# Performance work log

Hardware: AMD Instinct MI355X
Metric: run time of the kernel (lower is better)

## Reference

```python
import jax, jax.numpy as jnp
import numpy as np
import math

_B, _L, _D, _H = 4, 2048, 512, 8
_DH = _D // _H


def setup_inputs() -> dict:
    key = jax.random.key(0)
    ks = jax.random.split(key, 16)
    w_scale = 1.0 / math.sqrt(_D)
    def lin(kw, kb):
        W = jax.random.uniform(kw, (_D, _D), jnp.float32, -w_scale, w_scale)
        b = jax.random.uniform(kb, (_D,), jnp.float32, -w_scale, w_scale)
        return W, b
    Wq_w, Wq_b = lin(ks[0], ks[1])
    Wk_w, Wk_b = lin(ks[2], ks[3])
    Wv_w, Wv_b = lin(ks[4], ks[5])
    fc_w, fc_b = lin(ks[6], ks[7])
    Q = jax.random.normal(ks[8], (_B, _L, _D), jnp.float32)
    K = jax.random.normal(ks[9], (_B, _L, _D), jnp.float32)
    V = jax.random.normal(ks[10], (_B, _L, _D), jnp.float32)
    # E = torch.rand(L, DH): uniform [0,1), non-trainable buffer
    E = jax.random.uniform(ks[11], (_L, _DH), jnp.float32)
    # causal mask: True (1) where attention is disallowed -> gets -1e9
    mask = jnp.triu(jnp.ones((_L, _L), dtype=bool), k=1)[None, None]  # (1,1,L,L)
    return {"Q": Q, "K": K, "V": V, "mask": mask,
            "Wq_w": Wq_w, "Wq_b": Wq_b, "Wk_w": Wk_w, "Wk_b": Wk_b,
            "Wv_w": Wv_w, "Wv_b": Wv_b, "fc_w": fc_w, "fc_b": fc_b,
            "E": E, "H": _H}


def reference(Q, K, V, mask, Wq_w, Wq_b, Wk_w, Wk_b, Wv_w, Wv_b, fc_w, fc_b, E, H):
    B, Lq, D = Q.shape
    DH = D // H

    def proj(x, W, b):  # torch Linear: x @ W.T + b, then split heads -> (B,H,L,DH)
        y = x @ W.T + b
        return y.reshape(B, -1, H, DH).transpose(0, 2, 1, 3)

    q = proj(Q, Wq_w, Wq_b)
    k = proj(K, Wk_w, Wk_b)
    v = proj(V, Wv_w, Wv_b)
    Lk = k.shape[2]

    # _get_left_embedding: last Lq rows of E
    Eu = E[max(0, E.shape[0] - Lq):, :]            # (e, DH), e == Lq here
    e = Eu.shape[0]

    QE = jnp.einsum('bhld,ed->bhle', q, Eu)        # (B,H,Lq,e)
    # _qe_masking: keep QE[..., i, j] where j >= e-1-i (upper anti-triangle)
    i = jnp.arange(Lq)[:, None]
    j = jnp.arange(e)[None, :]
    keep = (i + j >= e - 1).astype(QE.dtype)
    QE = QE * keep

    # _skewing: pad one zero column, reshape, drop first row
    padded = jnp.pad(QE, ((0, 0), (0, 0), (0, 0), (1, 0)))   # (B,H,Lq,e+1)
    Srel = padded.reshape(B, H, e + 1, Lq)[:, :, 1:, :]      # (B,H,e,Lq)
    if Lk < Lq:
        Srel = Srel[:, :, :, :Lk]

    logits = (jnp.einsum('bhld,bhmd->bhlm', q, k) + Srel) / math.sqrt(DH)
    logits = logits + mask.astype(jnp.float32) * (-1e9)
    AW = jax.nn.softmax(logits, axis=-1)
    out = jnp.einsum('bhlm,bhmd->bhld', AW, v)               # (B,H,Lq,DH)
    out = out.transpose(0, 2, 1, 3).reshape(B, -1, D)        # (B,Lq,D)
    return out @ fc_w.T + fc_b
```

## Files before the change

### kernel.cpp

```cpp
#include <hip/hip_runtime.h>
#include <stdint.h>

typedef __bf16 bf16;
typedef float f32x4 __attribute__((ext_vector_type(4)));
typedef bf16 bf16x8 __attribute__((ext_vector_type(8)));
typedef bf16 bf16x4 __attribute__((ext_vector_type(4)));

#define MFMA16(a, b, c) __builtin_amdgcn_mfma_f32_16x16x32_bf16((a), (b), (c), 0, 0, 0)
#define EXP2F(x) __builtin_amdgcn_exp2f(x)

__device__ __forceinline__ void gll16(const void* g, void* l) {
  __builtin_amdgcn_global_load_lds((const __attribute__((address_space(1))) void*)g,
                                   (__attribute__((address_space(3))) void*)l, 16, 0, 0);
}

__global__ __launch_bounds__(256) void convert_all(
    const float4* __restrict__ Q, const float4* __restrict__ K, const float4* __restrict__ V,
    const float4* __restrict__ Wq, const float4* __restrict__ Wk, const float4* __restrict__ Wv,
    const float4* __restrict__ fcw, const float4* __restrict__ E,
    bf16x4* __restrict__ Xq, bf16x4* __restrict__ Xk, bf16x4* __restrict__ Xv,
    bf16x4* __restrict__ Wqb, bf16x4* __restrict__ Wkb, bf16x4* __restrict__ Wvb,
    bf16x4* __restrict__ fcb, bf16x4* __restrict__ Eb) {
  int i = blockIdx.x * 256 + threadIdx.x;
  const float4* s;
  bf16x4* d;
  int off;
  if (i < 1048576) { s = Q; d = Xq; off = i; }
  else if (i < 2097152) { s = K; d = Xk; off = i - 1048576; }
  else if (i < 3145728) { s = V; d = Xv; off = i - 2097152; }
  else if (i < 3211264) { s = Wq; d = Wqb; off = i - 3145728; }
  else if (i < 3276800) { s = Wk; d = Wkb; off = i - 3211264; }
  else if (i < 3342336) { s = Wv; d = Wvb; off = i - 3276800; }
  else if (i < 3407872) { s = fcw; d = fcb; off = i - 3342336; }
  else { s = E; d = Eb; off = i - 3407872; }
  float4 v = s[off];
  bf16x4 o;
  o[0] = (bf16)v.x; o[1] = (bf16)v.y; o[2] = (bf16)v.z; o[3] = (bf16)v.w;
  d[off] = o;
}

__device__ __forceinline__ void gemm_core64(const bf16* __restrict__ A,
                                            const bf16* __restrict__ Bt, bf16* ldsA,
                                            bf16* ldsB, int m0, int n0, f32x4 acc[4][2]) {
  const int t = threadIdx.x;
  const int lane = t & 63, w = t >> 6;
  const int l15 = lane & 15, quad = lane >> 4;
  const int wm = w >> 1, wn = w & 1;
#pragma unroll
  for (int i = 0; i < 4; i++)
#pragma unroll
    for (int j = 0; j < 2; j++) acc[i][j] = (f32x4){0.f, 0.f, 0.f, 0.f};

  const int r0 = t >> 2, c0 = (t & 3) ^ (r0 & 3);
  const int r1 = r0 + 64;

  int aoff[4], boff[2];
#pragma unroll
  for (int mt = 0; mt < 4; mt++) {
    int m = wm * 64 + mt * 16 + l15;
    aoff[mt] = (m << 6) + ((quad ^ (l15 & 3)) << 4);
  }
#pragma unroll
  for (int nt = 0; nt < 2; nt++) {
    int n = wn * 32 + nt * 16 + l15;
    boff[nt] = (n << 6) + ((quad ^ (l15 & 3)) << 4);
  }
  bf16* ldsA1 = ldsA + w * 512;
  bf16* ldsA2 = ldsA + 2048 + w * 512;
  bf16* ldsB1 = ldsB + w * 512;

  for (int kt = 0; kt < 512; kt += 32) {
    gll16(A + (size_t)(m0 + r0) * 512 + kt + c0 * 8, ldsA1);
    gll16(A + (size_t)(m0 + r1) * 512 + kt + c0 * 8, ldsA2);
    gll16(Bt + (size_t)(n0 + r0) * 512 + kt + c0 * 8, ldsB1);
    __syncthreads();
    bf16x8 af[4], bfr[2];
#pragma unroll
    for (int mt = 0; mt < 4; mt++) af[mt] = *(const bf16x8*)((const char*)ldsA + aoff[mt]);
#pragma unroll
    for (int nt = 0; nt < 2; nt++) bfr[nt] = *(const bf16x8*)((const char*)ldsB + boff[nt]);
#pragma unroll
    for (int mt = 0; mt < 4; mt++)
#pragma unroll
      for (int nt = 0; nt < 2; nt++)
        acc[mt][nt] = MFMA16(af[mt], bfr[nt], acc[mt][nt]);
    __syncthreads();
  }
}

__global__ __launch_bounds__(256) void proj_gemm(
    const bf16* __restrict__ Xq, const bf16* __restrict__ Xk, const bf16* __restrict__ Xv,
    const bf16* __restrict__ Wq, const bf16* __restrict__ Wk, const bf16* __restrict__ Wv,
    const float* __restrict__ bq, const float* __restrict__ bk, const float* __restrict__ bv,
    bf16* __restrict__ qb, bf16* __restrict__ kb, bf16* __restrict__ vT) {
  __shared__ __align__(16) char smem[17408];
  bf16* ldsA = (bf16*)smem;
  bf16* ldsB = (bf16*)(smem + 8192);
  const int z = blockIdx.z;
  const bf16* A = z == 0 ? Xq : (z == 1 ? Xk : Xv);
  const bf16* W = z == 0 ? Wq : (z == 1 ? Wk : Wv);
  const float* bias = z == 0 ? bq : (z == 1 ? bk : bv);
  const int m0 = blockIdx.x * 128, n0 = blockIdx.y * 64;
  f32x4 acc[4][2];
  gemm_core64(A, W, ldsA, ldsB, m0, n0, acc);

  const int t = threadIdx.x;
  const int lane = t & 63, w = t >> 6;
  const int l15 = lane & 15, quad = lane >> 4;
  const int wm = w >> 1, wn = w & 1;
  if (z == 2) {
    bf16* T = (bf16*)smem;
    const int b = m0 >> 11, l0 = m0 & 2047, h0 = blockIdx.y;
#pragma unroll
    for (int mt = 0; mt < 4; mt++)
#pragma unroll
      for (int nt = 0; nt < 2; nt++) {
        int d = wn * 32 + nt * 16 + l15;
        int lloc = wm * 64 + mt * 16 + quad * 4;
        float bi = bias[n0 + d];
        bf16x4 pv;
#pragma unroll
        for (int r = 0; r < 4; r++) pv[r] = (bf16)(acc[mt][nt][r] + bi);
        *(bf16x4*)&T[d * 136 + lloc] = pv;
      }
    __syncthreads();
    bf16* dsth = vT + ((size_t)((b * 8 + h0) * 64)) * 2048 + l0;
#pragma unroll
    for (int p = 0; p < 4; p++) {
      int id = t + 256 * p;
      int d = id >> 4, c = id & 15;
      bf16x8 v = *(const bf16x8*)&T[d * 136 + c * 8];
      *(bf16x8*)&dsth[(size_t)d * 2048 + c * 8] = v;
    }
  } else {
    bf16* out = z == 0 ? qb : kb;
#pragma unroll
    for (int mt = 0; mt < 4; mt++)
#pragma unroll
      for (int nt = 0; nt < 2; nt++)
#pragma unroll
        for (int r = 0; r < 4; r++) {
          int gm = m0 + wm * 64 + mt * 16 + quad * 4 + r;
          int gn = n0 + wn * 32 + nt * 16 + l15;
          float v = acc[mt][nt][r] + bias[gn];
          int b = gm >> 11, l = gm & 2047, h = gn >> 6, d = gn & 63;
          out[(((size_t)(b * 8 + h)) * 2048 + l) * 64 + d] = (bf16)v;
        }
  }
}

__global__ __launch_bounds__(256) void final_gemm(const bf16* __restrict__ A,
                                                  const bf16* __restrict__ W,
                                                  const float* __restrict__ bias,
                                                  float* __restrict__ out) {
  __shared__ __align__(16) char smem[12288];
  bf16* ldsA = (bf16*)smem;
  bf16* ldsB = (bf16*)(smem + 8192);
  const int m0 = blockIdx.x * 128, n0 = blockIdx.y * 64;
  f32x4 acc[4][2];
  gemm_core64(A, W, ldsA, ldsB, m0, n0, acc);

  const int t = threadIdx.x;
  const int lane = t & 63, w = t >> 6;
  const int l15 = lane & 15, quad = lane >> 4;
  const int wm = w >> 1, wn = w & 1;
#pragma unroll
  for (int mt = 0; mt < 4; mt++)
#pragma unroll
    for (int nt = 0; nt < 2; nt++)
#pragma unroll
      for (int r = 0; r < 4; r++) {
        int gm = m0 + wm * 64 + mt * 16 + quad * 4 + r;
        int gn = n0 + wn * 32 + nt * 16 + l15;
        out[(size_t)gm * 512 + gn] = acc[mt][nt][r] + bias[gn];
      }
}

__global__ __launch_bounds__(256, 4) void attn_kernel(
    const bf16* __restrict__ qbuf, const bf16* __restrict__ kbuf,
    const bf16* __restrict__ vT, const bf16* __restrict__ Eb,
    bf16* __restrict__ attnb, bf16* __restrict__ Of1,
    float* __restrict__ Os0, float* __restrict__ Os1) {
  __shared__ bf16 Kl[64 * 64];
  __shared__ bf16 Vl[64 * 64];
  __shared__ bf16 Pl[4][16 * 72];
  const int t = threadIdx.x, w = t >> 6, lane = t & 63;
  const int l15 = lane & 15, quad = lane >> 4;
  const int x = blockIdx.x;
  const int bh = x & 31, job = x >> 5;
  int strip, jt0, jt1;
  bool isB;
  if (job < 16) {
    strip = 16 + job; jt0 = 0; jt1 = 16; isB = false;
  } else {
    int k = job - 16, i = k >> 1;
    if ((k & 1) == 0) { strip = 15 - i; jt0 = 0; jt1 = 16 - i; isB = false; }
    else { strip = 31 - i; jt0 = 16; jt1 = 32 - i; isB = true; }
  }
  const int i0 = strip * 64 + w * 16;
  bf16* Pw = Pl[w];
  const bf16* qh = qbuf + (size_t)bh * 2048 * 64;
  const bf16* kh = kbuf + (size_t)bh * 2048 * 64;
  const bf16* vh = vT + (size_t)bh * 64 * 2048;

  const int sr0 = t >> 3, sc0 = (t & 7) ^ (sr0 & 7);
  const int sr1 = sr0 + 32;
  const int wb0 = (t & 192) * 16;
  const int wb1 = 4096 + wb0;

  int bpaddr[4];
  bool loA[4];
#pragma unroll
  for (int r = 0; r < 4; r++) {
    int u = quad * 4 + r;
    bpaddr[r] = (((l15 + 15 - u) & 15) + 16 * quad) * 4;
    loA[r] = (l15 <= u);
  }

  bf16x8 aq0, aq1;
  {
    const bf16* qrow = qh + (size_t)(i0 + l15) * 64 + quad * 8;
    aq0 = *(const bf16x8*)qrow;
    aq1 = *(const bf16x8*)(qrow + 32);
  }
  bf16x8 ones;
#pragma unroll
  for (int j = 0; j < 8; j++) ones[j] = (bf16)1.0f;

  f32x4 O[4], Osum;
  Osum = (f32x4){0.f, 0.f, 0.f, 0.f};
#pragma unroll
  for (int i = 0; i < 4; i++) O[i] = (f32x4){0.f, 0.f, 0.f, 0.f};
  const float sc = 0.125f * 1.44269504088896f;
  const int ebase00 = 2047 - i0 - 15;

  float Bpc[4];
  {
    int er = ebase00 + jt0 * 64 + l15;
    er = er > 2047 ? 2047 : er;
    const bf16* erow = Eb + (size_t)er * 64 + quad * 8;
    bf16x8 e0 = *(const bf16x8*)erow;
    bf16x8 e1 = *(const bf16x8*)(erow + 32);
    f32x4 zz = (f32x4){0.f, 0.f, 0.f, 0.f};
    zz = MFMA16(aq0, e0, zz);
    zz = MFMA16(aq1, e1, zz);
#pragma unroll
    for (int r = 0; r < 4; r++)
      Bpc[r] = __int_as_float(__builtin_amdgcn_ds_bpermute(bpaddr[r], __float_as_int(zz[r])));
  }

  for (int jt = jt0; jt < jt1; jt++) {
    const int j0 = jt * 64;
    const bool diag = (jt == strip);
    __syncthreads();
    gll16(kh + (size_t)(j0 + sr0) * 64 + sc0 * 8, (char*)Kl + wb0);
    gll16(kh + (size_t)(j0 + sr1) * 64 + sc0 * 8, (char*)Kl + wb1);
    gll16(vh + (size_t)sr0 * 2048 + j0 + sc0 * 8, (char*)Vl + wb0);
    gll16(vh + (size_t)sr1 * 2048 + j0 + sc0 * 8, (char*)Vl + wb1);
    float Bp[5][4];
#pragma unroll
    for (int r = 0; r < 4; r++) Bp[0][r] = Bpc[r];
    const int ebase = ebase00 + j0;
#pragma unroll
    for (int nt = 1; nt < 5; nt++) {
      int er = ebase + nt * 16 + l15;
      er = er > 2047 ? 2047 : er;
      const bf16* erow = Eb + (size_t)er * 64 + quad * 8;
      bf16x8 e0 = *(const bf16x8*)erow;
      bf16x8 e1 = *(const bf16x8*)(erow + 32);
      f32x4 zz = (f32x4){0.f, 0.f, 0.f, 0.f};
      zz = MFMA16(aq0, e0, zz);
      zz = MFMA16(aq1, e1, zz);
#pragma unroll
      for (int r = 0; r < 4; r++)
        Bp[nt][r] =
            __int_as_float(__builtin_amdgcn_ds_bpermute(bpaddr[r], __float_as_int(zz[r])));
    }
#pragma unroll
    for (int r = 0; r < 4; r++) Bpc[r] = Bp[4][r];

    __syncthreads();
    f32x4 s[4];
#pragma unroll
    for (int nt = 0; nt < 4; nt++) {
      int row = nt * 16 + l15;
      bf16x8 k0 = *(const bf16x8*)(Kl + ((row << 3) + (quad ^ (row & 7))) * 8);
      bf16x8 k1 = *(const bf16x8*)(Kl + ((row << 3) + ((quad + 4) ^ (row & 7))) * 8);
      f32x4 zz = (f32x4){0.f, 0.f, 0.f, 0.f};
      zz = MFMA16(aq0, k0, zz);
      s[nt] = MFMA16(aq1, k1, zz);
    }
    if (diag) {
#pragma unroll
      for (int nt = 0; nt < 4; nt++)
#pragma unroll
        for (int r = 0; r < 4; r++) {
          int u = quad * 4 + r;
          int j = nt * 16 + l15;
          float skew = loA[r] ? Bp[nt][r] : Bp[nt + 1][r];
          float logit = (s[nt][r] + skew) * sc;
          if (j0 + j > i0 + u) logit = -1e30f;
          Pw[u * 72 + j] = (bf16)EXP2F(logit);
        }
    } else {
#pragma unroll
      for (int nt = 0; nt < 4; nt++)
#pragma unroll
        for (int r = 0; r < 4; r++) {
          int u = quad * 4 + r;
          int j = nt * 16 + l15;
          float skew = loA[r] ? Bp[nt][r] : Bp[nt + 1][r];
          Pw[u * 72 + j] = (bf16)EXP2F((s[nt][r] + skew) * sc);
        }
    }
    bf16x8 pa0 = *(const bf16x8*)&Pw[l15 * 72 + quad * 8];
    bf16x8 pa1 = *(const bf16x8*)&Pw[l15 * 72 + 32 + quad * 8];
    Osum = MFMA16(pa0, ones, Osum);
    Osum = MFMA16(pa1, ones, Osum);
#pragma unroll
    for (int nt = 0; nt < 4; nt++) {
      int row = nt * 16 + l15;
      bf16x8 v0 = *(const bf16x8*)(Vl + ((row << 3) + (quad ^ (row & 7))) * 8);
      bf16x8 v1 = *(const bf16x8*)(Vl + ((row << 3) + ((quad + 4) ^ (row & 7))) * 8);
      O[nt] = MFMA16(pa0, v0, O[nt]);
      O[nt] = MFMA16(pa1, v1, O[nt]);
    }
  }
  if (isB) {
    bf16* orow = Of1 + ((size_t)(bh * 1024 + (i0 - 1024))) * 64;
#pragma unroll
    for (int nt = 0; nt < 4; nt++)
#pragma unroll
      for (int r = 0; r < 4; r++)
        orow[(size_t)(quad * 4 + r) * 64 + nt * 16 + l15] = (bf16)O[nt][r];
    if (l15 == 0) {
#pragma unroll
      for (int r = 0; r < 4; r++) Os1[bh * 1024 + (i0 - 1024) + quad * 4 + r] = Osum[r];
    }
  } else {
    const int b = bh >> 3, hh = bh & 7;
    bf16* orow = attnb + ((size_t)(b * 2048 + i0)) * 512 + hh * 64;
#pragma unroll
    for (int nt = 0; nt < 4; nt++)
#pragma unroll
      for (int r = 0; r < 4; r++)
        orow[(size_t)(quad * 4 + r) * 512 + nt * 16 + l15] = (bf16)O[nt][r];
    if (l15 == 0) {
#pragma unroll
      for (int r = 0; r < 4; r++) Os0[bh * 2048 + i0 + quad * 4 + r] = Osum[r];
    }
  }
}

__global__ __launch_bounds__(256) void norm_kernel(bf16x8* __restrict__ attnb,
                                                   const bf16x8* __restrict__ Of1,
                                                   const float* __restrict__ Os0,
                                                   const float* __restrict__ Os1) {
  int i = blockIdx.x * 256 + threadIdx.x;
  int col8 = i & 63;
  int row = i >> 6;
  int b = row >> 11, l = row & 2047, h = col8 >> 3;
  int bh = b * 8 + h;
  float s = Os0[bh * 2048 + l];
  bf16x8 v0 = attnb[i];
  float acc[8];
#pragma unroll
  for (int j = 0; j < 8; j++) acc[j] = (float)v0[j];
  if (l >= 1024) {
    s += Os1[bh * 1024 + l - 1024];
    bf16x8 v1 = Of1[(size_t)(bh * 1024 + l - 1024) * 8 + (col8 & 7)];
#pragma unroll
    for (int j = 0; j < 8; j++) acc[j] += (float)v1[j];
  }
  float inv = 1.0f / s;
  bf16x8 o;
#pragma unroll
  for (int j = 0; j < 8; j++) o[j] = (bf16)(acc[j] * inv);
  attnb[i] = o;
}

extern "C" void kernel_launch(void* const* d_in, const int* in_sizes, int n_in,
                              void* d_out, int out_size, void* d_ws, size_t ws_size,
                              hipStream_t stream) {
  const float* Q = (const float*)d_in[0];
  const float* K = (const float*)d_in[1];
  const float* V = (const float*)d_in[2];
  const float* Wq = (const float*)d_in[4];
  const float* bq = (const float*)d_in[5];
  const float* Wk = (const float*)d_in[6];
  const float* bk = (const float*)d_in[7];
  const float* Wv = (const float*)d_in[8];
  const float* bv = (const float*)d_in[9];
  const float* fcw = (const float*)d_in[10];
  const float* fcb = (const float*)d_in[11];
  const float* E = (const float*)d_in[12];

  char* ws = (char*)d_ws;
  bf16* Xq = (bf16*)(ws + 0);
  bf16* Xk = (bf16*)(ws + 8388608);
  bf16* Xv = (bf16*)(ws + 16777216);
  bf16* Wqb = (bf16*)(ws + 25165824);
  bf16* Wkb = (bf16*)(ws + 25690112);
  bf16* Wvb = (bf16*)(ws + 26214400);
  bf16* fcwb = (bf16*)(ws + 26738688);
  bf16* Eb = (bf16*)(ws + 27262976);
  bf16* qbuf = (bf16*)(ws + 27525120);
  bf16* kbuf = (bf16*)(ws + 35913728);
  bf16* vTb = (bf16*)(ws + 44302336);
  bf16* Of1 = (bf16*)(ws + 52690944);
  float* Os0 = (float*)(ws + 56885248);
  float* Os1 = (float*)(ws + 57147392);
  bf16* attnb = Xq;

  convert_all<<<13440, 256, 0, stream>>>(
      (const float4*)Q, (const float4*)K, (const float4*)V, (const float4*)Wq,
      (const float4*)Wk, (const float4*)Wv, (const float4*)fcw, (const float4*)E,
      (bf16x4*)Xq, (bf16x4*)Xk, (bf16x4*)Xv, (bf16x4*)Wqb, (bf16x4*)Wkb,
      (bf16x4*)Wvb, (bf16x4*)fcwb, (bf16x4*)Eb);

  proj_gemm<<<dim3(64, 8, 3), 256, 0, stream>>>(Xq, Xk, Xv, Wqb, Wkb, Wvb, bq, bk, bv,
                                                qbuf, kbuf, vTb);

  attn_kernel<<<1536, 256, 0, stream>>>(qbuf, kbuf, vTb, Eb, attnb, Of1, Os0, Os1);

  norm_kernel<<<2048, 256, 0, stream>>>((bf16x8*)attnb, (const bf16x8*)Of1, Os0, Os1);

  final_gemm<<<dim3(64, 8), 256, 0, stream>>>(attnb, fcwb, fcb, (float*)d_out);
}
```

Measured before the change: 244.1 us.

## Fuse fp32-to-bf16 input conversion into projection GEMM and shrink normalization pass

The projection GEMM now loads the fp32 Q/K/V activations straight into LDS and converts them to bf16 while building MFMA fragments. This removes the separate conversion pass that read and wrote about 24 MB of bf16 copies. Attention strips that are not split across jobs now normalize their output in the epilogue, so the norm kernel only handles the split rows (the second half of each sequence). The final GEMM uses 64x64 tiles to launch more blocks. In exchange, fp32 tiles double the LDS traffic per K-step in the projection, and the conversion work now sits inside the GEMM inner loop.

```diff
diff --git a/kernel.cpp b/kernel.cpp
--- a/kernel.cpp
+++ b/kernel.cpp
@@ -14,71 +14,80 @@
                                    (__attribute__((address_space(3))) void*)l, 16, 0, 0);
 }
 
-__global__ __launch_bounds__(256) void convert_all(
-    const float4* __restrict__ Q, const float4* __restrict__ K, const float4* __restrict__ V,
-    const float4* __restrict__ Wq, const float4* __restrict__ Wk, const float4* __restrict__ Wv,
-    const float4* __restrict__ fcw, const float4* __restrict__ E,
-    bf16x4* __restrict__ Xq, bf16x4* __restrict__ Xk, bf16x4* __restrict__ Xv,
-    bf16x4* __restrict__ Wqb, bf16x4* __restrict__ Wkb, bf16x4* __restrict__ Wvb,
-    bf16x4* __restrict__ fcb, bf16x4* __restrict__ Eb) {
+__global__ __launch_bounds__(256) void convert_we(
+    const float4* __restrict__ Wq, const float4* __restrict__ Wk,
+    const float4* __restrict__ Wv, const float4* __restrict__ fcw,
+    const float4* __restrict__ E, bf16x4* __restrict__ Wqb, bf16x4* __restrict__ Wkb,
+    bf16x4* __restrict__ Wvb, bf16x4* __restrict__ fcb, bf16x4* __restrict__ Eb) {
   int i = blockIdx.x * 256 + threadIdx.x;
   const float4* s;
   bf16x4* d;
   int off;
-  if (i < 1048576) { s = Q; d = Xq; off = i; }
-  else if (i < 2097152) { s = K; d = Xk; off = i - 1048576; }
-  else if (i < 3145728) { s = V; d = Xv; off = i - 2097152; }
-  else if (i < 3211264) { s = Wq; d = Wqb; off = i - 3145728; }
-  else if (i < 3276800) { s = Wk; d = Wkb; off = i - 3211264; }
-  else if (i < 3342336) { s = Wv; d = Wvb; off = i - 3276800; }
-  else if (i < 3407872) { s = fcw; d = fcb; off = i - 3342336; }
-  else { s = E; d = Eb; off = i - 3407872; }
+  if (i < 65536) { s = Wq; d = Wqb; off = i; }
+  else if (i < 131072) { s = Wk; d = Wkb; off = i - 65536; }
+  else if (i < 196608) { s = Wv; d = Wvb; off = i - 131072; }
+  else if (i < 262144) { s = fcw; d = fcb; off = i - 196608; }
+  else { s = E; d = Eb; off = i - 262144; }
   float4 v = s[off];
   bf16x4 o;
   o[0] = (bf16)v.x; o[1] = (bf16)v.y; o[2] = (bf16)v.z; o[3] = (bf16)v.w;
   d[off] = o;
 }
 
-__device__ __forceinline__ void gemm_core64(const bf16* __restrict__ A,
-                                            const bf16* __restrict__ Bt, bf16* ldsA,
-                                            bf16* ldsB, int m0, int n0, f32x4 acc[4][2]) {
+__global__ __launch_bounds__(256) void proj_gemm(
+    const float* __restrict__ Q, const float* __restrict__ K, const float* __restrict__ V,
+    const bf16* __restrict__ Wq, const bf16* __restrict__ Wk, const bf16* __restrict__ Wv,
+    const float* __restrict__ bq, const float* __restrict__ bk, const float* __restrict__ bv,
+    bf16* __restrict__ qb, bf16* __restrict__ kb, bf16* __restrict__ vT) {
+  __shared__ __align__(16) char smem[20480];
+  char* ldsA = smem;
+  char* ldsB = smem + 16384;
+  const int z = blockIdx.z;
+  const float* A = z == 0 ? Q : (z == 1 ? K : V);
+  const bf16* W = z == 0 ? Wq : (z == 1 ? Wk : Wv);
+  const float* bias = z == 0 ? bq : (z == 1 ? bk : bv);
+  const int m0 = blockIdx.x * 128, n0 = blockIdx.y * 64;
   const int t = threadIdx.x;
   const int lane = t & 63, w = t >> 6;
   const int l15 = lane & 15, quad = lane >> 4;
   const int wm = w >> 1, wn = w & 1;
+  f32x4 acc[4][2];
 #pragma unroll
   for (int i = 0; i < 4; i++)
 #pragma unroll
     for (int j = 0; j < 2; j++) acc[i][j] = (f32x4){0.f, 0.f, 0.f, 0.f};
 
-  const int r0 = t >> 2, c0 = (t & 3) ^ (r0 & 3);
-  const int r1 = r0 + 64;
-
-  int aoff[4], boff[2];
-#pragma unroll
-  for (int mt = 0; mt < 4; mt++) {
-    int m = wm * 64 + mt * 16 + l15;
-    aoff[mt] = (m << 6) + ((quad ^ (l15 & 3)) << 4);
-  }
+  const int ar = t >> 3, ac = (t & 7) ^ (ar & 7);
+  const int br = t >> 2, bc = (t & 3) ^ (br & 3);
+  const int wbase = (t & 192) * 16;
+
+  int boff[2];
 #pragma unroll
   for (int nt = 0; nt < 2; nt++) {
     int n = wn * 32 + nt * 16 + l15;
-    boff[nt] = (n << 6) + ((quad ^ (l15 & 3)) << 4);
-  }
-  bf16* ldsA1 = ldsA + w * 512;
-  bf16* ldsA2 = ldsA + 2048 + w * 512;
-  bf16* ldsB1 = ldsB + w * 512;
+    boff[nt] = (n << 6) + ((quad ^ (n & 3)) << 4);
+  }
 
   for (int kt = 0; kt < 512; kt += 32) {
-    gll16(A + (size_t)(m0 + r0) * 512 + kt + c0 * 8, ldsA1);
-    gll16(A + (size_t)(m0 + r1) * 512 + kt + c0 * 8, ldsA2);
-    gll16(Bt + (size_t)(n0 + r0) * 512 + kt + c0 * 8, ldsB1);
+#pragma unroll
+    for (int p = 0; p < 4; p++)
+      gll16(A + (size_t)(m0 + ar + 32 * p) * 512 + kt + ac * 4, ldsA + p * 4096 + wbase);
+    gll16(W + (size_t)(n0 + br) * 512 + kt + bc * 8, ldsB + wbase);
     __syncthreads();
     bf16x8 af[4], bfr[2];
 #pragma unroll
-    for (int mt = 0; mt < 4; mt++) af[mt] = *(const bf16x8*)((const char*)ldsA + aoff[mt]);
-#pragma unroll
-    for (int nt = 0; nt < 2; nt++) bfr[nt] = *(const bf16x8*)((const char*)ldsB + boff[nt]);
+    for (int mt = 0; mt < 4; mt++) {
+      int m = wm * 64 + mt * 16 + l15;
+      const char* base = ldsA + (m << 7);
+      float4 x0 = *(const float4*)(base + ((((quad << 1) | 0) ^ (m & 7)) << 4));
+      float4 x1 = *(const float4*)(base + ((((quad << 1) | 1) ^ (m & 7)) << 4));
+      bf16x8 v;
+      v[0] = (bf16)x0.x; v[1] = (bf16)x0.y; v[2] = (bf16)x0.z; v[3] = (bf16)x0.w;
+      v[4] = (bf16)x1.x; v[5] = (bf16)x1.y; v[6] = (bf16)x1.z; v[7] = (bf16)x1.w;
+      af[mt] = v;
+    }
+#pragma unroll
+    for (int nt = 0; nt < 2; nt++) bfr[nt] = *(const bf16x8*)(ldsB + boff[nt]);
 #pragma unroll
     for (int mt = 0; mt < 4; mt++)
 #pragma unroll
@@ -86,28 +95,7 @@
         acc[mt][nt] = MFMA16(af[mt], bfr[nt], acc[mt][nt]);
     __syncthreads();
   }
-}
-
-__global__ __launch_bounds__(256) void proj_gemm(
-    const bf16* __restrict__ Xq, const bf16* __restrict__ Xk, const bf16* __restrict__ Xv,
-    const bf16* __restrict__ Wq, const bf16* __restrict__ Wk, const bf16* __restrict__ Wv,
-    const float* __restrict__ bq, const float* __restrict__ bk, const float* __restrict__ bv,
-    bf16* __restrict__ qb, bf16* __restrict__ kb, bf16* __restrict__ vT) {
-  __shared__ __align__(16) char smem[17408];
-  bf16* ldsA = (bf16*)smem;
-  bf16* ldsB = (bf16*)(smem + 8192);
-  const int z = blockIdx.z;
-  const bf16* A = z == 0 ? Xq : (z == 1 ? Xk : Xv);
-  const bf16* W = z == 0 ? Wq : (z == 1 ? Wk : Wv);
-  const float* bias = z == 0 ? bq : (z == 1 ? bk : bv);
-  const int m0 = blockIdx.x * 128, n0 = blockIdx.y * 64;
-  f32x4 acc[4][2];
-  gemm_core64(A, W, ldsA, ldsB, m0, n0, acc);
-
-  const int t = threadIdx.x;
-  const int lane = t & 63, w = t >> 6;
-  const int l15 = lane & 15, quad = lane >> 4;
-  const int wm = w >> 1, wn = w & 1;
+
   if (z == 2) {
     bf16* T = (bf16*)smem;
     const int b = m0 >> 11, l0 = m0 & 2047, h0 = blockIdx.y;
@@ -153,24 +141,55 @@
                                                   const bf16* __restrict__ W,
                                                   const float* __restrict__ bias,
                                                   float* __restrict__ out) {
-  __shared__ __align__(16) char smem[12288];
-  bf16* ldsA = (bf16*)smem;
-  bf16* ldsB = (bf16*)(smem + 8192);
-  const int m0 = blockIdx.x * 128, n0 = blockIdx.y * 64;
-  f32x4 acc[4][2];
-  gemm_core64(A, W, ldsA, ldsB, m0, n0, acc);
-
+  __shared__ __align__(16) bf16 ldsA[64 * 32];
+  __shared__ __align__(16) bf16 ldsB[64 * 32];
+  const int m0 = blockIdx.x * 64, n0 = blockIdx.y * 64;
   const int t = threadIdx.x;
   const int lane = t & 63, w = t >> 6;
   const int l15 = lane & 15, quad = lane >> 4;
   const int wm = w >> 1, wn = w & 1;
-#pragma unroll
-  for (int mt = 0; mt < 4; mt++)
+  f32x4 acc[2][2];
+#pragma unroll
+  for (int i = 0; i < 2; i++)
+#pragma unroll
+    for (int j = 0; j < 2; j++) acc[i][j] = (f32x4){0.f, 0.f, 0.f, 0.f};
+
+  const int r0 = t >> 2, c0 = (t & 3) ^ (r0 & 3);
+  const int wbase = (t & 192) * 16;
+
+  int aoff[2], boff[2];
+#pragma unroll
+  for (int mt = 0; mt < 2; mt++) {
+    int m = wm * 32 + mt * 16 + l15;
+    aoff[mt] = (m << 6) + ((quad ^ (m & 3)) << 4);
+    int n = wn * 32 + mt * 16 + l15;
+    boff[mt] = (n << 6) + ((quad ^ (n & 3)) << 4);
+  }
+
+  for (int kt = 0; kt < 512; kt += 32) {
+    gll16(A + (size_t)(m0 + r0) * 512 + kt + c0 * 8, (char*)ldsA + wbase);
+    gll16(W + (size_t)(n0 + r0) * 512 + kt + c0 * 8, (char*)ldsB + wbase);
+    __syncthreads();
+    bf16x8 af[2], bfr[2];
+#pragma unroll
+    for (int mt = 0; mt < 2; mt++) af[mt] = *(const bf16x8*)((const char*)ldsA + aoff[mt]);
+#pragma unroll
+    for (int nt = 0; nt < 2; nt++) bfr[nt] = *(const bf16x8*)((const char*)ldsB + boff[nt]);
+#pragma unroll
+    for (int mt = 0; mt < 2; mt++)
+#pragma unroll
+      for (int nt = 0; nt < 2; nt++)
+        acc[mt][nt] = MFMA16(af[mt], bfr[nt], acc[mt][nt]);
+    __syncthreads();
+  }
+
+#pragma unroll
+  for (int mt = 0; mt < 2; mt++)
 #pragma unroll
     for (int nt = 0; nt < 2; nt++)
 #pragma unroll
       for (int r = 0; r < 4; r++) {
-        int gm = m0 + wm * 64 + mt * 16 + quad * 4 + r;
+        int gm = m0 + wm * 32 + mt * 16 + quad * 4 + r;
         int gn = n0 + wn * 32 + nt * 16 + l15;
         out[(size_t)gm * 512 + gn] = acc[mt][nt][r] + bias[gn];
       }
@@ -337,6 +356,17 @@
 #pragma unroll
       for (int r = 0; r < 4; r++) Os1[bh * 1024 + (i0 - 1024) + quad * 4 + r] = Osum[r];
     }
+  } else if (strip < 16) {
+    const int b = bh >> 3, hh = bh & 7;
+    bf16* orow = attnb + ((size_t)(b * 2048 + i0)) * 512 + hh * 64;
+    float inv[4];
+#pragma unroll
+    for (int r = 0; r < 4; r++) inv[r] = 1.0f / Osum[r];
+#pragma unroll
+    for (int nt = 0; nt < 4; nt++)
+#pragma unroll
+      for (int r = 0; r < 4; r++)
+        orow[(size_t)(quad * 4 + r) * 512 + nt * 16 + l15] = (bf16)(O[nt][r] * inv[r]);
   } else {
     const int b = bh >> 3, hh = bh & 7;
     bf16* orow = attnb + ((size_t)(b * 2048 + i0)) * 512 + hh * 64;
@@ -358,25 +388,19 @@
                                                    const float* __restrict__ Os1) {
   int i = blockIdx.x * 256 + threadIdx.x;
   int col8 = i & 63;
-  int row = i >> 6;
-  int b = row >> 11, l = row & 2047, h = col8 >> 3;
+  int rid = i >> 6;
+  int b = rid >> 10, lo = rid & 1023;
+  int h = col8 >> 3, c8 = col8 & 7;
   int bh = b * 8 + h;
-  float s = Os0[bh * 2048 + l];
-  bf16x8 v0 = attnb[i];
-  float acc[8];
-#pragma unroll
-  for (int j = 0; j < 8; j++) acc[j] = (float)v0[j];
-  if (l >= 1024) {
-    s += Os1[bh * 1024 + l - 1024];
-    bf16x8 v1 = Of1[(size_t)(bh * 1024 + l - 1024) * 8 + (col8 & 7)];
-#pragma unroll
-    for (int j = 0; j < 8; j++) acc[j] += (float)v1[j];
-  }
+  float s = Os0[bh * 2048 + 1024 + lo] + Os1[bh * 1024 + lo];
+  size_t ai = ((size_t)(b * 2048 + 1024 + lo)) * 64 + col8;
+  bf16x8 v0 = attnb[ai];
+  bf16x8 v1 = Of1[(size_t)(bh * 1024 + lo) * 8 + c8];
   float inv = 1.0f / s;
   bf16x8 o;
 #pragma unroll
-  for (int j = 0; j < 8; j++) o[j] = (bf16)(acc[j] * inv);
-  attnb[i] = o;
+  for (int j = 0; j < 8; j++) o[j] = (bf16)(((float)v0[j] + (float)v1[j]) * inv);
+  attnb[ai] = o;
 }
 
 extern "C" void kernel_launch(void* const* d_in, const int* in_sizes, int n_in,
@@ -396,9 +420,6 @@
   const float* E = (const float*)d_in[12];
 
   char* ws = (char*)d_ws;
-  bf16* Xq = (bf16*)(ws + 0);
-  bf16* Xk = (bf16*)(ws + 8388608);
-  bf16* Xv = (bf16*)(ws + 16777216);
   bf16* Wqb = (bf16*)(ws + 25165824);
   bf16* Wkb = (bf16*)(ws + 25690112);
   bf16* Wvb = (bf16*)(ws + 26214400);
@@ -410,20 +431,19 @@
   bf16* Of1 = (bf16*)(ws + 52690944);
   float* Os0 = (float*)(ws + 56885248);
   float* Os1 = (float*)(ws + 57147392);
-  bf16* attnb = Xq;
-
-  convert_all<<<13440, 256, 0, stream>>>(
-      (const float4*)Q, (const float4*)K, (const float4*)V, (const float4*)Wq,
-      (const float4*)Wk, (const float4*)Wv, (const float4*)fcw, (const float4*)E,
-      (bf16x4*)Xq, (bf16x4*)Xk, (bf16x4*)Xv, (bf16x4*)Wqb, (bf16x4*)Wkb,
-      (bf16x4*)Wvb, (bf16x4*)fcwb, (bf16x4*)Eb);
-
-  proj_gemm<<<dim3(64, 8, 3), 256, 0, stream>>>(Xq, Xk, Xv, Wqb, Wkb, Wvb, bq, bk, bv,
+  bf16* attnb = (bf16*)(ws + 0);
+
+  convert_we<<<1152, 256, 0, stream>>>(
+      (const float4*)Wq, (const float4*)Wk, (const float4*)Wv, (const float4*)fcw,
+      (const float4*)E, (bf16x4*)Wqb, (bf16x4*)Wkb, (bf16x4*)Wvb, (bf16x4*)fcwb,
+      (bf16x4*)Eb);
+
+  proj_gemm<<<dim3(64, 8, 3), 256, 0, stream>>>(Q, K, V, Wqb, Wkb, Wvb, bq, bk, bv,
                                                 qbuf, kbuf, vTb);
 
   attn_kernel<<<1536, 256, 0, stream>>>(qbuf, kbuf, vTb, Eb, attnb, Of1, Os0, Os1);
 
-  norm_kernel<<<2048, 256, 0, stream>>>((bf16x8*)attnb, (const bf16x8*)Of1, Os0, Os1);
-
-  final_gemm<<<dim3(64, 8), 256, 0, stream>>>(attnb, fcwb, fcb, (float*)d_out);
-}
+  norm_kernel<<<1024, 256, 0, stream>>>((bf16x8*)attnb, (const bf16x8*)Of1, Os0, Os1);
+
+  final_gemm<<<dim3(128, 8), 256, 0, stream>>>(attnb, fcwb, fcb, (float*)d_out);
+}
```

Measured after the change: 251.7 us. 1.03x slower.

## Normalize short attention strips in-kernel and shrink final GEMM tiles

Applied to the files above, without the earlier changes.

Attention rows in the first half (strip < 16, not split across two jobs) are now divided by their softmax sum directly in the attention kernel, so the normalization kernel only processes the second half of rows that need merging of two partial results. This halves the norm kernel's memory traffic and grid. Separately, the final projection GEMM switches from 128x64 tiles using the shared core to a dedicated 64x64 tile loop with direct global-to-LDS loads, doubling the block count for better CU occupancy at the cost of more redundant weight loads and a non-double-buffered K loop with two barriers per step.

```diff
diff --git a/kernel.cpp b/kernel.cpp
--- a/kernel.cpp
+++ b/kernel.cpp
@@ -153,24 +153,55 @@
                                                   const bf16* __restrict__ W,
                                                   const float* __restrict__ bias,
                                                   float* __restrict__ out) {
-  __shared__ __align__(16) char smem[12288];
-  bf16* ldsA = (bf16*)smem;
-  bf16* ldsB = (bf16*)(smem + 8192);
-  const int m0 = blockIdx.x * 128, n0 = blockIdx.y * 64;
-  f32x4 acc[4][2];
-  gemm_core64(A, W, ldsA, ldsB, m0, n0, acc);
-
+  __shared__ __align__(16) bf16 ldsA[64 * 32];
+  __shared__ __align__(16) bf16 ldsB[64 * 32];
+  const int m0 = blockIdx.x * 64, n0 = blockIdx.y * 64;
   const int t = threadIdx.x;
   const int lane = t & 63, w = t >> 6;
   const int l15 = lane & 15, quad = lane >> 4;
   const int wm = w >> 1, wn = w & 1;
-#pragma unroll
-  for (int mt = 0; mt < 4; mt++)
+  f32x4 acc[2][2];
+#pragma unroll
+  for (int i = 0; i < 2; i++)
+#pragma unroll
+    for (int j = 0; j < 2; j++) acc[i][j] = (f32x4){0.f, 0.f, 0.f, 0.f};
+
+  const int r0 = t >> 2, c0 = (t & 3) ^ (r0 & 3);
+  const int wbase = (t & 192) * 16;
+
+  int aoff[2], boff[2];
+#pragma unroll
+  for (int mt = 0; mt < 2; mt++) {
+    int m = wm * 32 + mt * 16 + l15;
+    aoff[mt] = (m << 6) + ((quad ^ (m & 3)) << 4);
+    int n = wn * 32 + mt * 16 + l15;
+    boff[mt] = (n << 6) + ((quad ^ (n & 3)) << 4);
+  }
+
+  for (int kt = 0; kt < 512; kt += 32) {
+    gll16(A + (size_t)(m0 + r0) * 512 + kt + c0 * 8, (char*)ldsA + wbase);
+    gll16(W + (size_t)(n0 + r0) * 512 + kt + c0 * 8, (char*)ldsB + wbase);
+    __syncthreads();
+    bf16x8 af[2], bfr[2];
+#pragma unroll
+    for (int mt = 0; mt < 2; mt++) af[mt] = *(const bf16x8*)((const char*)ldsA + aoff[mt]);
+#pragma unroll
+    for (int nt = 0; nt < 2; nt++) bfr[nt] = *(const bf16x8*)((const char*)ldsB + boff[nt]);
+#pragma unroll
+    for (int mt = 0; mt < 2; mt++)
+#pragma unroll
+      for (int nt = 0; nt < 2; nt++)
+        acc[mt][nt] = MFMA16(af[mt], bfr[nt], acc[mt][nt]);
+    __syncthreads();
+  }
+
+#pragma unroll
+  for (int mt = 0; mt < 2; mt++)
 #pragma unroll
     for (int nt = 0; nt < 2; nt++)
 #pragma unroll
       for (int r = 0; r < 4; r++) {
-        int gm = m0 + wm * 64 + mt * 16 + quad * 4 + r;
+        int gm = m0 + wm * 32 + mt * 16 + quad * 4 + r;
         int gn = n0 + wn * 32 + nt * 16 + l15;
         out[(size_t)gm * 512 + gn] = acc[mt][nt][r] + bias[gn];
       }
@@ -337,6 +368,17 @@
 #pragma unroll
       for (int r = 0; r < 4; r++) Os1[bh * 1024 + (i0 - 1024) + quad * 4 + r] = Osum[r];
     }
+  } else if (strip < 16) {
+    const int b = bh >> 3, hh = bh & 7;
+    bf16* orow = attnb + ((size_t)(b * 2048 + i0)) * 512 + hh * 64;
+    float inv[4];
+#pragma unroll
+    for (int r = 0; r < 4; r++) inv[r] = 1.0f / Osum[r];
+#pragma unroll
+    for (int nt = 0; nt < 4; nt++)
+#pragma unroll
+      for (int r = 0; r < 4; r++)
+        orow[(size_t)(quad * 4 + r) * 512 + nt * 16 + l15] = (bf16)(O[nt][r] * inv[r]);
   } else {
     const int b = bh >> 3, hh = bh & 7;
     bf16* orow = attnb + ((size_t)(b * 2048 + i0)) * 512 + hh * 64;
@@ -358,25 +400,19 @@
                                                    const float* __restrict__ Os1) {
   int i = blockIdx.x * 256 + threadIdx.x;
   int col8 = i & 63;
-  int row = i >> 6;
-  int b = row >> 11, l = row & 2047, h = col8 >> 3;
+  int rid = i >> 6;
+  int b = rid >> 10, lo = rid & 1023;
+  int h = col8 >> 3, c8 = col8 & 7;
   int bh = b * 8 + h;
-  float s = Os0[bh * 2048 + l];
-  bf16x8 v0 = attnb[i];
-  float acc[8];
-#pragma unroll
-  for (int j = 0; j < 8; j++) acc[j] = (float)v0[j];
-  if (l >= 1024) {
-    s += Os1[bh * 1024 + l - 1024];
-    bf16x8 v1 = Of1[(size_t)(bh * 1024 + l - 1024) * 8 + (col8 & 7)];
-#pragma unroll
-    for (int j = 0; j < 8; j++) acc[j] += (float)v1[j];
-  }
+  float s = Os0[bh * 2048 + 1024 + lo] + Os1[bh * 1024 + lo];
+  size_t ai = ((size_t)(b * 2048 + 1024 + lo)) * 64 + col8;
+  bf16x8 v0 = attnb[ai];
+  bf16x8 v1 = Of1[(size_t)(bh * 1024 + lo) * 8 + c8];
   float inv = 1.0f / s;
   bf16x8 o;
 #pragma unroll
-  for (int j = 0; j < 8; j++) o[j] = (bf16)(acc[j] * inv);
-  attnb[i] = o;
+  for (int j = 0; j < 8; j++) o[j] = (bf16)(((float)v0[j] + (float)v1[j]) * inv);
+  attnb[ai] = o;
 }
 
 extern "C" void kernel_launch(void* const* d_in, const int* in_sizes, int n_in,
@@ -423,7 +459,7 @@
 
   attn_kernel<<<1536, 256, 0, stream>>>(qbuf, kbuf, vTb, Eb, attnb, Of1, Os0, Os1);
 
-  norm_kernel<<<2048, 256, 0, stream>>>((bf16x8*)attnb, (const bf16x8*)Of1, Os0, Os1);
-
-  final_gemm<<<dim3(64, 8), 256, 0, stream>>>(attnb, fcwb, fcb, (float*)d_out);
-}
+  norm_kernel<<<1024, 256, 0, stream>>>((bf16x8*)attnb, (const bf16x8*)Of1, Os0, Os1);
+
+  final_gemm<<<dim3(128, 8), 256, 0, stream>>>(attnb, fcwb, fcb, (float*)d_out);
+}
```

Result: no change. 243.0 us (-0.4%).
